# Kernel optimization log

Hardware: AMD Instinct MI355X
Metric: run time of the kernel (lower is better)

Reference implementation:

```python
import jax, jax.numpy as jnp
import numpy as np

NUM_HEADS = 16  # from init_kwargs


def setup_inputs() -> dict:
    key = jax.random.key(0)
    k1, k2, k3, k4, k5 = jax.random.split(key, 5)
    B, N, C = 2, 2048, 1024
    return {
        "query": jax.random.normal(k1, (B, N, C), dtype=jnp.float32),
        "key": jax.random.normal(k2, (B, N, C), dtype=jnp.float32),
        "value": jax.random.normal(k3, (B, N, C), dtype=jnp.float32),
        "W_merge": jax.random.normal(k4, (C, C), dtype=jnp.float32) * (1.0 / np.sqrt(C)),
        "b_merge": jax.random.normal(k5, (C,), dtype=jnp.float32) * 0.02,
    }


def reference(query, key, value, W_merge, b_merge):
    B, N, C = query.shape
    H = NUM_HEADS
    dim = C // H
    # Faithful to torch: plain reshape (B,N,C) -> (B, dim, H, N), no transpose.
    q = query.reshape(B, dim, H, -1)
    k = key.reshape(B, dim, H, -1)
    v = value.reshape(B, dim, H, -1)
    # Faithful scale: divide by sqrt(N) (sequence length), as in the source.
    scale = 1.0 / np.sqrt(N).astype(np.float32)
    scores = jnp.einsum('bdhn,bdhm->bhnm', q, k) * scale  # [B,H,N,N]
    attn = jax.nn.softmax(scores, axis=-1)
    x = jnp.einsum('bhnm,bdhm->bdhn', attn, v)  # [B,dim,H,N]
    x = x.reshape(B, C, -1)  # [B,C,N]
    # Conv1d(C,C,kernel_size=1) == pointwise channel matmul + bias
    out = jnp.einsum('oc,bcn->bon', W_merge, x) + b_merge[None, :, None]
    return out  # [B,C,N]
```

## Files before the change

### kernel.cpp

```cpp
#include <hip/hip_runtime.h>


#define H 16
#define NSEQ 2048
#define CCH 1024
#define BATCH 2
#define DSTR (H * NSEQ)

typedef __attribute__((ext_vector_type(8))) short bf16x8;
typedef __attribute__((ext_vector_type(2))) float f32x2;
typedef __attribute__((ext_vector_type(4))) float f32x4;
typedef __attribute__((ext_vector_type(16))) float f32x16;
typedef __attribute__((ext_vector_type(4))) unsigned int uint32x4;

__device__ __forceinline__ unsigned short f2bf(float x) {
  unsigned int u = __builtin_bit_cast(unsigned int, x);
  u += 0x7FFFu + ((u >> 16) & 1u);
  return (unsigned short)(u >> 16);
}

__device__ __forceinline__ unsigned int pack2bf(float a, float b) {
#if __has_builtin(__builtin_amdgcn_cvt_pk_bf16_f32)
  typedef __attribute__((ext_vector_type(2))) __bf16 bf16x2_t;
  bf16x2_t r = __builtin_amdgcn_cvt_pk_bf16_f32(a, b);
  return __builtin_bit_cast(unsigned int, r);
#else
  unsigned int ua = __builtin_bit_cast(unsigned int, a);
  unsigned int ub = __builtin_bit_cast(unsigned int, b);
  ua += 0x7FFFu + ((ua >> 16) & 1u);
  ub += 0x7FFFu + ((ub >> 16) & 1u);
  return __builtin_amdgcn_perm(ub, ua, 0x07060302u);
#endif
}

__device__ __forceinline__ float fast_exp2(float x) {
#if __has_builtin(__builtin_amdgcn_exp2f)
  return __builtin_amdgcn_exp2f(x);
#else
  return exp2f(x);
#endif
}

__device__ __forceinline__ void permswap32(unsigned int& a, unsigned int& b) {
#if __has_builtin(__builtin_amdgcn_permlane32_swap)
  typedef __attribute__((ext_vector_type(2))) unsigned int uint2v;
  uint2v r = __builtin_amdgcn_permlane32_swap(a, b, false, false);
  a = r[0];
  b = r[1];
#else
  unsigned int ax = (unsigned int)__shfl_xor((int)a, 32, 64);
  unsigned int bx = (unsigned int)__shfl_xor((int)b, 32, 64);
  bool lo = (threadIdx.x & 63) < 32;
  unsigned int na = lo ? a : bx;
  unsigned int nb = lo ? ax : b;
  a = na;
  b = nb;
#endif
}

__device__ __forceinline__ void gld16(const void* g, void* l) {
  __builtin_amdgcn_global_load_lds(
      (const __attribute__((address_space(1))) unsigned int*)g,
      (__attribute__((address_space(3))) unsigned int*)l, 16, 0, 0);
}

__device__ __forceinline__ f32x16 zero16() {
  f32x16 v;
#pragma unroll
  for (int i = 0; i < 16; ++i) v[i] = 0.f;
  return v;
}

__global__ __launch_bounds__(256) void prep_all(const float* __restrict__ W,
                                                const float* __restrict__ v,
                                                const float* __restrict__ q,
                                                const float* __restrict__ k,
                                                unsigned short* __restrict__ Wp,
                                                unsigned short* __restrict__ VB,
                                                unsigned short* __restrict__ Qt,
                                                unsigned short* __restrict__ KA) {
  __shared__ unsigned short T[64][72];
  __shared__ unsigned short VL[256 * 8];
  const int bid = blockIdx.x, tid = threadIdx.x;

  if (bid < 1024) {
    const int o = bid;
    const int cp = tid * 4;
    const int hh = cp >> 6;
    const int d0 = cp & 63;
    const float* Wr = W + (size_t)o * CCH;
    ushort4 ov;
    ov.x = f2bf(Wr[(d0 + 0) * H + hh]);
    ov.y = f2bf(Wr[(d0 + 1) * H + hh]);
    ov.z = f2bf(Wr[(d0 + 2) * H + hh]);
    ov.w = f2bf(Wr[(d0 + 3) * H + hh]);
    *(ushort4*)&Wp[(size_t)o * CCH + cp] = ov;
  } else if (bid < 3072) {
    const int vb = bid - 1024;
    const int bh = vb >> 6, kbb = vb & 63;
    const int bb = bh >> 4, hhh = bh & 15;
    const int d = tid >> 2, nq = (tid & 3) * 8;
    const float* srcv =
        v + (size_t)bb * (CCH * NSEQ) + (size_t)d * DSTR + hhh * NSEQ + kbb * 32 + nq;
    float4 x0 = *(const float4*)srcv;
    float4 x1 = *(const float4*)(srcv + 4);
    unsigned short* Lc = &VL[tid * 8];
    Lc[0] = f2bf(x0.x); Lc[1] = f2bf(x0.y); Lc[2] = f2bf(x0.z); Lc[3] = f2bf(x0.w);
    Lc[4] = f2bf(x1.x); Lc[5] = f2bf(x1.y); Lc[6] = f2bf(x1.z); Lc[7] = f2bf(x1.w);
    __syncthreads();
    const int kb_lo = tid >> 6, d2 = tid & 63;
    *(bf16x8*)(VB + (size_t)bh * 131072 + (size_t)(kbb * 4 + kb_lo) * 512 + d2 * 8) =
        *(const bf16x8*)&VL[(d2 * 4 + kb_lo) * 8];
  } else {
    const int lbid = bid - 3072;
    const int n0 = (lbid & 31) * 64;
    const int hh = (lbid >> 5) & 15;
    const int zz = lbid >> 9;
    const int b = zz >> 1, t = zz & 1;
    const float* src = t ? k : q;
    const float scl = t ? 1.0f : (0.022097086912079608f * 1.4426950408889634f);
    const size_t base = (size_t)b * (CCH * NSEQ) + (size_t)hh * NSEQ;
#pragma unroll
    for (int it = 0; it < 4; ++it) {
      int i4 = it * 256 + tid;
      int d = i4 >> 4;
      int nn = (i4 & 15) << 2;
      float4 val = *(const float4*)(src + base + (size_t)d * DSTR + n0 + nn);
      T[nn + 0][d] = f2bf(val.x * scl);
      T[nn + 1][d] = f2bf(val.y * scl);
      T[nn + 2][d] = f2bf(val.z * scl);
      T[nn + 3][d] = f2bf(val.w * scl);
    }
    __syncthreads();
    if (t == 0) {
      const size_t obase = ((size_t)(b * H + hh) * NSEQ + n0) * 64;
#pragma unroll
      for (int it = 0; it < 2; ++it) {
        int idx = it * 256 + tid;
        int row = idx >> 3, cb = idx & 7;
        *(bf16x8*)(Qt + obase + (size_t)row * 64 + cb * 8) = *(const bf16x8*)&T[row][cb * 8];
      }
    } else {
      const size_t obase = (size_t)(b * H + hh) * 131072 + (size_t)(n0 >> 5) * 2048;
#pragma unroll
      for (int it = 0; it < 2; ++it) {
        int idx = it * 256 + tid;
        int nl = idx >> 3, sub = idx & 7;
        *(bf16x8*)(KA + obase + (size_t)(nl >> 5) * 2048 + sub * 256 + (nl & 31) * 8) =
            *(const bf16x8*)&T[nl][sub * 8];
      }
    }
  }
}


__device__ __forceinline__ void exppack(const f32x16& St, f32x2& ls2, bf16x8& a0, bf16x8& a1) {
  unsigned int pd[8];
#pragma unroll
  for (int t = 0; t < 8; ++t) {
    float e0 = fast_exp2(St[2 * t]);
    float e1 = fast_exp2(St[2 * t + 1]);
    ls2 += (f32x2){e0, e1};
    pd[t] = pack2bf(e0, e1);
  }
  unsigned int s0[4] = {pd[0], pd[1], pd[2], pd[3]};
  unsigned int s1[4] = {pd[4], pd[5], pd[6], pd[7]};
  permswap32(s0[0], s0[2]);
  permswap32(s0[1], s0[3]);
  permswap32(s1[0], s1[2]);
  permswap32(s1[1], s1[3]);
  a0 = __builtin_bit_cast(bf16x8, (uint32x4){s0[0], s0[1], s0[2], s0[3]});
  a1 = __builtin_bit_cast(bf16x8, (uint32x4){s1[0], s1[1], s1[2], s1[3]});
}

__global__ __launch_bounds__(512, 4) void attn9(const unsigned short* __restrict__ Qt,
                                                const unsigned short* __restrict__ KA,
                                                const unsigned short* __restrict__ VB,
                                                unsigned short* __restrict__ xt) {
  __shared__ __align__(16) float eplds[128 * 64 + 256];
  float* Oex = eplds;
  float* lsumLDS = eplds + 8192;

  const int tid = threadIdx.x;
  const int w = tid >> 6, lane = tid & 63;
  const int lane31 = lane & 31, hl = lane >> 5;
  const int g = w >> 2, nw = w & 3;
  const int n0 = blockIdx.x * 128;
  const int hh = blockIdx.y, b = blockIdx.z;
  const int bh = b * H + hh;

  bf16x8 bQ[4];
  const unsigned short* Qb = Qt + ((size_t)bh * NSEQ + n0 + nw * 32 + lane31) * 64;
#pragma unroll
  for (int ks = 0; ks < 4; ++ks) bQ[ks] = *(const bf16x8*)(Qb + (ks * 2 + hl) * 8);

  const unsigned short* kp = KA + (size_t)bh * 131072 + g * 65536 + hl * 256 + lane31 * 8;
  const unsigned short* vp = VB + (size_t)bh * 131072 + g * 65536 + hl * 512 + lane31 * 8;

  f32x16 O[2];
  O[0] = zero16();
  O[1] = zero16();
  f32x2 ls2 = {0.f, 0.f};

#define LOADK(R0, R1, R2, R3, C)                      \
  {                                                   \
    const unsigned short* kc_ = kp + (C)*2048;        \
    R0 = *(const bf16x8*)(kc_);                       \
    R1 = *(const bf16x8*)(kc_ + 512);                 \
    R2 = *(const bf16x8*)(kc_ + 1024);                \
    R3 = *(const bf16x8*)(kc_ + 1536);                \
  }

#define CHUNK(K0, K1, K2, K3, C)                                                \
  {                                                                             \
    __builtin_amdgcn_s_setprio(1);                                              \
    f32x16 St = zero16();                                                       \
    St = __builtin_amdgcn_mfma_f32_32x32x16_bf16(K0, bQ[0], St, 0, 0, 0);       \
    St = __builtin_amdgcn_mfma_f32_32x32x16_bf16(K1, bQ[1], St, 0, 0, 0);       \
    St = __builtin_amdgcn_mfma_f32_32x32x16_bf16(K2, bQ[2], St, 0, 0, 0);       \
    St = __builtin_amdgcn_mfma_f32_32x32x16_bf16(K3, bQ[3], St, 0, 0, 0);       \
    __builtin_amdgcn_s_setprio(0);                                              \
    bf16x8 a0, a1;                                                              \
    exppack(St, ls2, a0, a1);                                                   \
    const unsigned short* vc_ = vp + (C)*2048;                                  \
    bf16x8 v00 = *(const bf16x8*)(vc_);                                         \
    bf16x8 v01 = *(const bf16x8*)(vc_ + 256);                                   \
    bf16x8 v10 = *(const bf16x8*)(vc_ + 1024);                                  \
    bf16x8 v11 = *(const bf16x8*)(vc_ + 1280);                                  \
    __builtin_amdgcn_s_setprio(1);                                              \
    O[0] = __builtin_amdgcn_mfma_f32_32x32x16_bf16(a0, v00, O[0], 0, 0, 0);     \
    O[1] = __builtin_amdgcn_mfma_f32_32x32x16_bf16(a0, v01, O[1], 0, 0, 0);     \
    O[0] = __builtin_amdgcn_mfma_f32_32x32x16_bf16(a1, v10, O[0], 0, 0, 0);     \
    O[1] = __builtin_amdgcn_mfma_f32_32x32x16_bf16(a1, v11, O[1], 0, 0, 0);     \
    __builtin_amdgcn_s_setprio(0);                                              \
  }

  bf16x8 kA0, kA1, kA2, kA3, kB0, kB1, kB2, kB3;
  LOADK(kA0, kA1, kA2, kA3, 0);
  for (int j = 0; j < 16; ++j) {
    LOADK(kB0, kB1, kB2, kB3, 2 * j + 1);
    CHUNK(kA0, kA1, kA2, kA3, 2 * j);
    LOADK(kA0, kA1, kA2, kA3, 2 * j + 2);
    CHUNK(kB0, kB1, kB2, kB3, 2 * j + 1);
    if ((j & 3) == 3) __syncthreads();
  }
#undef CHUNK
#undef LOADK

  float lsum = ls2[0] + ls2[1];
  lsum += __shfl_xor(lsum, 32, 64);
  if (hl == 0) lsumLDS[g * 128 + nw * 32 + lane31] = lsum;
  if (g == 1) {
#pragma unroll
    for (int dt = 0; dt < 2; ++dt)
#pragma unroll
      for (int r = 0; r < 16; ++r) {
        int nl = nw * 32 + (r & 3) + 8 * (r >> 2) + 4 * hl;
        Oex[nl * 64 + dt * 32 + lane31] = O[dt][r];
      }
  }
  __syncthreads();
  if (g == 0) {
    const size_t xb = (size_t)b * ((size_t)NSEQ * CCH);
#pragma unroll
    for (int rq = 0; rq < 4; ++rq) {
      int nlb = nw * 32 + rq * 8 + 4 * hl;
      float4 l0 = *(const float4*)&lsumLDS[nlb];
      float4 l1 = *(const float4*)&lsumLDS[128 + nlb];
      float inv0 = 1.0f / (l0.x + l1.x);
      float inv1 = 1.0f / (l0.y + l1.y);
      float inv2 = 1.0f / (l0.z + l1.z);
      float inv3 = 1.0f / (l0.w + l1.w);
#pragma unroll
      for (int dt = 0; dt < 2; ++dt) {
        int d = dt * 32 + lane31;
#pragma unroll
        for (int rr = 0; rr < 4; ++rr) {
          int r = rq * 4 + rr;
          float val = O[dt][r] + Oex[(nlb + rr) * 64 + d];
          float inv = (rr == 0) ? inv0 : (rr == 1) ? inv1 : (rr == 2) ? inv2 : inv3;
          int n = n0 + nlb + rr;
          xt[xb + (size_t)n * CCH + hh * 64 + d] = f2bf(val * inv);
        }
      }
    }
  }
}

__global__ __launch_bounds__(256) void merge5(const unsigned short* __restrict__ Wp,
                                              const unsigned short* __restrict__ xt,
                                              const float* __restrict__ bias,
                                              float* __restrict__ out) {
  __shared__ unsigned short At[2][64 * 64];
  __shared__ unsigned short Bt[2][64 * 64];
  const int tid = threadIdx.x;
  const int w = tid >> 6, lane = tid & 63;
  const int quad = lane >> 4, l16 = lane & 15;
  const int wx = w & 1, wy = w >> 1;
  const int n0 = blockIdx.x * 64, o0 = blockIdx.y * 64, b = blockIdx.z;
  const int srow = w * 8 + (lane >> 3), scb = lane & 7;
  const unsigned short* Bbase = xt + (size_t)b * ((size_t)NSEQ * CCH);

  f32x4 acc[2][2];
#pragma unroll
  for (int ot = 0; ot < 2; ++ot)
#pragma unroll
    for (int nt = 0; nt < 2; ++nt) acc[ot][nt] = (f32x4){0.f, 0.f, 0.f, 0.f};

#pragma unroll
  for (int i = 0; i < 2; ++i) {
    int row = i * 32 + srow;
    int cbl = scb ^ (row & 7);
    gld16(Wp + (size_t)(o0 + row) * CCH + cbl * 8, &At[0][(i * 32 + w * 8) * 64]);
    gld16(Bbase + (size_t)(n0 + row) * CCH + cbl * 8, &Bt[0][(i * 32 + w * 8) * 64]);
  }
  __syncthreads();

  for (int it = 0; it < 16; ++it) {
    const int cur = it & 1;
    if (it < 15) {
      const int nxt = cur ^ 1;
      const int c0 = (it + 1) * 64;
#pragma unroll
      for (int i = 0; i < 2; ++i) {
        int row = i * 32 + srow;
        int cbl = scb ^ (row & 7);
        gld16(Wp + (size_t)(o0 + row) * CCH + c0 + cbl * 8, &At[nxt][(i * 32 + w * 8) * 64]);
        gld16(Bbase + (size_t)(n0 + row) * CCH + c0 + cbl * 8, &Bt[nxt][(i * 32 + w * 8) * 64]);
      }
    }
#pragma unroll
    for (int ks = 0; ks < 2; ++ks) {
      int phys = ((ks * 4 + quad) ^ (l16 & 7)) * 8;
      bf16x8 aW[2], bX[2];
#pragma unroll
      for (int ot = 0; ot < 2; ++ot)
        aW[ot] = *(const bf16x8*)&At[cur][(wy * 32 + ot * 16 + l16) * 64 + phys];
#pragma unroll
      for (int nt = 0; nt < 2; ++nt)
        bX[nt] = *(const bf16x8*)&Bt[cur][(wx * 32 + nt * 16 + l16) * 64 + phys];
#pragma unroll
      for (int ot = 0; ot < 2; ++ot)
#pragma unroll
        for (int nt = 0; nt < 2; ++nt)
          acc[ot][nt] =
              __builtin_amdgcn_mfma_f32_16x16x32_bf16(aW[ot], bX[nt], acc[ot][nt], 0, 0, 0);
    }
    __syncthreads();
  }

#pragma unroll
  for (int ot = 0; ot < 2; ++ot) {
#pragma unroll
    for (int r = 0; r < 4; ++r) {
      int o = o0 + wy * 32 + ot * 16 + quad * 4 + r;
      float br = bias[o];
#pragma unroll
      for (int nt = 0; nt < 2; ++nt)
        out[(size_t)b * ((size_t)CCH * NSEQ) + (size_t)o * NSEQ + n0 + wx * 32 + nt * 16 + l16] =
            acc[ot][nt][r] + br;
    }
  }
}

extern "C" void kernel_launch(void* const* d_in, const int* in_sizes, int n_in,
                              void* d_out, int out_size, void* d_ws, size_t ws_size,
                              hipStream_t stream) {
  const float* q = (const float*)d_in[0];
  const float* k = (const float*)d_in[1];
  const float* v = (const float*)d_in[2];
  const float* W = (const float*)d_in[3];
  const float* bias = (const float*)d_in[4];
  float* out = (float*)d_out;

  unsigned short* Wp = (unsigned short*)d_ws;
  unsigned short* xt = Wp + (1u << 20);
  unsigned short* Qt = xt + (4u << 20);
  unsigned short* KA = Qt + (4u << 20);
  unsigned short* VB = KA + (4u << 20);

  hipLaunchKernelGGL(prep_all, dim3(5120), dim3(256), 0, stream, W, v, q, k, Wp, VB, Qt, KA);
  hipLaunchKernelGGL(attn9, dim3(NSEQ / 128, H, BATCH), dim3(512), 0, stream, Qt, KA, VB, xt);
  hipLaunchKernelGGL(merge5, dim3(NSEQ / 64, CCH / 64, BATCH), dim3(256), 0, stream,
                     Wp, xt, bias, out);
}
```

Baseline: 162.6 us.

## Triple-buffer merge GEMM with single barrier and coalesce W permutation via LDS

The merge GEMM moves from a double-buffered loop with two barriers per iteration to a three-stage ring buffer. It uses an explicit vmcnt wait and one barrier per K step, which lets global-to-LDS loads run two stages ahead of the MFMA work. Separately, the weight permutation in the prep kernel now reads each W row with coalesced float4 loads and transposes through a small LDS tile, replacing the strided scalar gathers. The trade-off is more LDS per block for the merge kernel, and correctness now depends on hand-set waitcnt values.

```diff
diff --git a/kernel.cpp b/kernel.cpp
--- a/kernel.cpp
+++ b/kernel.cpp
@@ -81,20 +81,26 @@
                                                 unsigned short* __restrict__ KA) {
   __shared__ unsigned short T[64][72];
   __shared__ unsigned short VL[256 * 8];
+  __shared__ unsigned short Tw[16][72];
   const int bid = blockIdx.x, tid = threadIdx.x;
 
   if (bid < 1024) {
     const int o = bid;
-    const int cp = tid * 4;
-    const int hh = cp >> 6;
-    const int d0 = cp & 63;
     const float* Wr = W + (size_t)o * CCH;
-    ushort4 ov;
-    ov.x = f2bf(Wr[(d0 + 0) * H + hh]);
-    ov.y = f2bf(Wr[(d0 + 1) * H + hh]);
-    ov.z = f2bf(Wr[(d0 + 2) * H + hh]);
-    ov.w = f2bf(Wr[(d0 + 3) * H + hh]);
-    *(ushort4*)&Wp[(size_t)o * CCH + cp] = ov;
+    float4 x = *(const float4*)(Wr + tid * 4);
+    {
+      int c = tid * 4;
+      Tw[c & 15][c >> 4] = f2bf(x.x);
+      c++;
+      Tw[c & 15][c >> 4] = f2bf(x.y);
+      c++;
+      Tw[c & 15][c >> 4] = f2bf(x.z);
+      c++;
+      Tw[c & 15][c >> 4] = f2bf(x.w);
+    }
+    __syncthreads();
+    const int cp = tid * 4, hh = cp >> 6, d0 = cp & 63;
+    *(ushort4*)&Wp[(size_t)o * CCH + cp] = *(const ushort4*)&Tw[hh][d0];
   } else if (bid < 3072) {
     const int vb = bid - 1024;
     const int bh = vb >> 6, kbb = vb & 63;
@@ -287,12 +293,12 @@
   }
 }
 
-__global__ __launch_bounds__(256) void merge5(const unsigned short* __restrict__ Wp,
+__global__ __launch_bounds__(256) void merge6(const unsigned short* __restrict__ Wp,
                                               const unsigned short* __restrict__ xt,
                                               const float* __restrict__ bias,
                                               float* __restrict__ out) {
-  __shared__ unsigned short At[2][64 * 64];
-  __shared__ unsigned short Bt[2][64 * 64];
+  __shared__ unsigned short At[3][64 * 64];
+  __shared__ unsigned short Bt[3][64 * 64];
   const int tid = threadIdx.x;
   const int w = tid >> 6, lane = tid & 63;
   const int quad = lane >> 4, l16 = lane & 15;
@@ -307,47 +313,50 @@
 #pragma unroll
     for (int nt = 0; nt < 2; ++nt) acc[ot][nt] = (f32x4){0.f, 0.f, 0.f, 0.f};
 
-#pragma unroll
-  for (int i = 0; i < 2; ++i) {
-    int row = i * 32 + srow;
-    int cbl = scb ^ (row & 7);
-    gld16(Wp + (size_t)(o0 + row) * CCH + cbl * 8, &At[0][(i * 32 + w * 8) * 64]);
-    gld16(Bbase + (size_t)(n0 + row) * CCH + cbl * 8, &Bt[0][(i * 32 + w * 8) * 64]);
-  }
-  __syncthreads();
-
-  for (int it = 0; it < 16; ++it) {
-    const int cur = it & 1;
-    if (it < 15) {
-      const int nxt = cur ^ 1;
-      const int c0 = (it + 1) * 64;
-#pragma unroll
-      for (int i = 0; i < 2; ++i) {
-        int row = i * 32 + srow;
-        int cbl = scb ^ (row & 7);
-        gld16(Wp + (size_t)(o0 + row) * CCH + c0 + cbl * 8, &At[nxt][(i * 32 + w * 8) * 64]);
-        gld16(Bbase + (size_t)(n0 + row) * CCH + c0 + cbl * 8, &Bt[nxt][(i * 32 + w * 8) * 64]);
-      }
-    }
-#pragma unroll
-    for (int ks = 0; ks < 2; ++ks) {
-      int phys = ((ks * 4 + quad) ^ (l16 & 7)) * 8;
-      bf16x8 aW[2], bX[2];
-#pragma unroll
-      for (int ot = 0; ot < 2; ++ot)
-        aW[ot] = *(const bf16x8*)&At[cur][(wy * 32 + ot * 16 + l16) * 64 + phys];
-#pragma unroll
-      for (int nt = 0; nt < 2; ++nt)
-        bX[nt] = *(const bf16x8*)&Bt[cur][(wx * 32 + nt * 16 + l16) * 64 + phys];
-#pragma unroll
-      for (int ot = 0; ot < 2; ++ot)
-#pragma unroll
-        for (int nt = 0; nt < 2; ++nt)
-          acc[ot][nt] =
-              __builtin_amdgcn_mfma_f32_16x16x32_bf16(aW[ot], bX[nt], acc[ot][nt], 0, 0, 0);
-    }
-    __syncthreads();
-  }
+#define STG(BUF, C0)                                                           \
+  {                                                                            \
+    _Pragma("unroll") for (int i = 0; i < 2; ++i) {                            \
+      int row = i * 32 + srow;                                                 \
+      int cbl = scb ^ (row & 7);                                               \
+      gld16(Wp + (size_t)(o0 + row) * CCH + (C0) + cbl * 8,                    \
+            &At[BUF][(i * 32 + w * 8) * 64]);                                  \
+      gld16(Bbase + (size_t)(n0 + row) * CCH + (C0) + cbl * 8,                 \
+            &Bt[BUF][(i * 32 + w * 8) * 64]);                                  \
+    }                                                                          \
+  }
+
+#define CMP(CUR)                                                               \
+  {                                                                            \
+    const unsigned short* Ac = &At[0][0] + (CUR)*4096;                         \
+    const unsigned short* Bc = &Bt[0][0] + (CUR)*4096;                         \
+    _Pragma("unroll") for (int ks = 0; ks < 2; ++ks) {                         \
+      int phys = ((ks * 4 + quad) ^ (l16 & 7)) * 8;                            \
+      bf16x8 aW[2], bX[2];                                                     \
+      _Pragma("unroll") for (int ot = 0; ot < 2; ++ot)                         \
+          aW[ot] = *(const bf16x8*)&Ac[(wy * 32 + ot * 16 + l16) * 64 + phys]; \
+      _Pragma("unroll") for (int nt = 0; nt < 2; ++nt)                         \
+          bX[nt] = *(const bf16x8*)&Bc[(wx * 32 + nt * 16 + l16) * 64 + phys]; \
+      _Pragma("unroll") for (int ot = 0; ot < 2; ++ot)                         \
+          _Pragma("unroll") for (int nt = 0; nt < 2; ++nt) acc[ot][nt] =       \
+              __builtin_amdgcn_mfma_f32_16x16x32_bf16(aW[ot], bX[nt],          \
+                                                      acc[ot][nt], 0, 0, 0);   \
+    }                                                                          \
+  }
+
+  STG(0, 0);
+  STG(1, 64);
+  for (int it = 0; it < 15; ++it) {
+    const int cur = it % 3;
+    asm volatile("s_waitcnt vmcnt(4)" ::: "memory");
+    __builtin_amdgcn_s_barrier();
+    if (it < 14) STG((it + 2) % 3, (it + 2) * 64);
+    CMP(cur);
+  }
+  asm volatile("s_waitcnt vmcnt(0)" ::: "memory");
+  __builtin_amdgcn_s_barrier();
+  CMP(0);
+#undef CMP
+#undef STG
 
 #pragma unroll
   for (int ot = 0; ot < 2; ++ot) {
@@ -381,6 +390,6 @@
 
   hipLaunchKernelGGL(prep_all, dim3(5120), dim3(256), 0, stream, W, v, q, k, Wp, VB, Qt, KA);
   hipLaunchKernelGGL(attn9, dim3(NSEQ / 128, H, BATCH), dim3(512), 0, stream, Qt, KA, VB, xt);
-  hipLaunchKernelGGL(merge5, dim3(NSEQ / 64, CCH / 64, BATCH), dim3(256), 0, stream,
+  hipLaunchKernelGGL(merge6, dim3(NSEQ / 64, CCH / 64, BATCH), dim3(256), 0, stream,
                      Wp, xt, bias, out);
 }
```

Result: slower. 165.9 us (+2.0%).
